# Kernel optimization log

Measured on AMD Instinct MI355X. Metric: run time of the kernel, lower is better.

Reference implementation:

```python
import jax, jax.numpy as jnp
import numpy as np

D_OUT = 256  # out_channels; fourier dim F = D_OUT (Wr has F/2 rows)

def _fourier_pos(H, W, Wr, w1, b1, w2, b2):
    # normalized (H,W) grid in [-1,1], shape [L,2]
    ys = jnp.linspace(-1.0, 1.0, H)
    xs = jnp.linspace(-1.0, 1.0, W)
    gy, gx = jnp.meshgrid(ys, xs, indexing='ij')
    grid = jnp.stack([gy, gx], axis=-1).reshape(-1, 2)  # [L,2]
    proj = grid @ Wr.T                                   # [L,F/2]
    F = 2 * Wr.shape[0]
    feats = jnp.concatenate([jnp.cos(proj), jnp.sin(proj)], axis=-1) / jnp.sqrt(jnp.float32(F))
    h = jax.nn.gelu(feats @ w1.T + b1)
    return h @ w2.T + b2                                 # [L,D_OUT]

def setup_inputs() -> dict:
    key = jax.random.key(0)
    ks = jax.random.split(key, 11)
    N, D, H, W = 16, 256, 128, 128
    s = 1.0 / np.sqrt(D)
    return {
        'x': jax.random.normal(ks[0], (N, D, H, W), jnp.float32),
        'query': jax.random.normal(ks[1], (D_OUT,), jnp.float32),
        'k_w': jax.random.normal(ks[2], (D_OUT, D), jnp.float32) * s,
        'k_b': jax.random.normal(ks[3], (D_OUT,), jnp.float32) * 0.01,
        'v_w': jax.random.normal(ks[4], (D_OUT, D), jnp.float32) * s,
        'v_b': jax.random.normal(ks[5], (D_OUT,), jnp.float32) * 0.01,
        'Wr': jax.random.normal(ks[6], (D_OUT // 2, 2), jnp.float32),
        'w1': jax.random.normal(ks[7], (D_OUT, D_OUT), jnp.float32) * (1.0 / np.sqrt(D_OUT)),
        'b1': jax.random.normal(ks[8], (D_OUT,), jnp.float32) * 0.01,
        'w2': jax.random.normal(ks[9], (D_OUT, D_OUT), jnp.float32) * (1.0 / np.sqrt(D_OUT)),
        'b2': jax.random.normal(ks[10], (D_OUT,), jnp.float32) * 0.01,
    }

def reference(x, query, k_w, k_b, v_w, v_b, Wr, w1, b1, w2, b2):
    N, D, H, W = x.shape
    L = H * W
    tok = x.reshape(N, D, L).transpose(0, 2, 1)          # [N,L,D]
    pos = _fourier_pos(H, W, Wr, w1, b1, w2, b2)         # [L,D_OUT]
    K = tok @ k_w.T + k_b + pos[None]                    # [N,L,D_OUT]
    V = tok @ v_w.T + v_b                                # [N,L,D_OUT]
    scores = jnp.einsum('nld,d->nl', K, query) / jnp.sqrt(jnp.float32(query.shape[0]))
    attn = jax.nn.softmax(scores, axis=1)                # [N,L]
    return jnp.einsum('nl,nld->nd', attn, V)             # [N,D_OUT]
```

## Files before the change

### kernel.cpp

```cpp
#include <hip/hip_runtime.h>
#include <math.h>

#define NB 16
#define DD 256
#define LL 16384
#define DO 256

#define WS_QK    0
#define WS_QW2   256
#define WS_C1    512
#define WS_C2    513
#define WS_W1T   768
#define WS_VWT   (WS_W1T + 65536)
#define WS_PQ    (WS_VWT + 65536)
#define WS_M     (WS_PQ + LL)
#define WS_DEN   (WS_M + NB*32)
#define WS_NUM   (WS_DEN + NB*32)

__device__ __forceinline__ float gelu_tanh(float u) {
    float u3 = u*u*u;
    return 0.5f*u*(1.0f + tanhf(0.7978845608028654f*(u + 0.044715f*u3)));
}

__global__ __launch_bounds__(256) void k0a(const float* __restrict__ query,
        const float* __restrict__ k_w, const float* __restrict__ k_b,
        const float* __restrict__ w2, const float* __restrict__ b2,
        float* __restrict__ ws) {
    __shared__ float q_s[DO];
    __shared__ float red[256];
    int t = threadIdx.x;
    q_s[t] = query[t];
    __syncthreads();
    float aqk = 0.f, aqw = 0.f;
    for (int o = 0; o < DO; ++o) {
        aqk += k_w[o*DD + t] * q_s[o];
        aqw += w2[o*DO + t] * q_s[o];
    }
    ws[WS_QK + t] = aqk;
    ws[WS_QW2 + t] = aqw;
    red[t] = k_b[t]*q_s[t];
    __syncthreads();
    for (int s = 128; s > 0; s >>= 1) { if (t < s) red[t] += red[t+s]; __syncthreads(); }
    if (t == 0) ws[WS_C1] = red[0];
    __syncthreads();
    red[t] = b2[t]*q_s[t];
    __syncthreads();
    for (int s = 128; s > 0; s >>= 1) { if (t < s) red[t] += red[t+s]; __syncthreads(); }
    if (t == 0) ws[WS_C2] = red[0];
}

__global__ __launch_bounds__(256) void k0b(const float* __restrict__ w1,
        const float* __restrict__ v_w, float* __restrict__ ws) {
    int t = threadIdx.x, b = blockIdx.x;
    if (b < 256) {
        ws[WS_W1T + b*DO + t] = w1[t*DO + b];
    } else {
        int c = b - 256;
        ws[WS_VWT + c*DO + t] = v_w[t*DD + c];
    }
}

__global__ __launch_bounds__(256) void k1_pq(const float* __restrict__ Wr,
        const float* __restrict__ b1, float* __restrict__ ws) {
    __shared__ float feats[32*256];
    __shared__ float wbuf[32*256];
    int t = threadIdx.x;
    int w = t >> 6, lane = t & 63;
    int l0 = blockIdx.x * 32;
    int r = t & 127;
    float wr0 = Wr[r*2], wr1 = Wr[r*2+1];
    bool is_cos = (t < 128);
    for (int lr = 0; lr < 32; ++lr) {
        int l = l0 + lr;
        int i = l >> 7, j = l & 127;
        float y = -1.0f + (2.0f/127.0f)*(float)i;
        float xg = -1.0f + (2.0f/127.0f)*(float)j;
        float p = y*wr0 + xg*wr1;
        feats[lr*256 + t] = (is_cos ? cosf(p) : sinf(p)) * 0.0625f;
    }
    int o4 = lane * 4;
    float z[8][4];
    #pragma unroll
    for (int a = 0; a < 8; ++a) { z[a][0]=0.f; z[a][1]=0.f; z[a][2]=0.f; z[a][3]=0.f; }
    __syncthreads();
    for (int fc = 0; fc < 8; ++fc) {
        #pragma unroll
        for (int i2 = 0; i2 < 8; ++i2) {
            int idx = i2*256 + t;
            int fl = idx >> 6;
            int c = (idx & 63) * 4;
            *(float4*)(wbuf + fl*256 + c) =
                *(const float4*)(ws + WS_W1T + (fc*32+fl)*DO + c);
        }
        __syncthreads();
        for (int f = 0; f < 32; ++f) {
            float4 wv = *(const float4*)(wbuf + f*256 + o4);
            #pragma unroll
            for (int lr = 0; lr < 8; ++lr) {
                float fv = feats[(w*8+lr)*256 + fc*32 + f];
                z[lr][0] += fv*wv.x; z[lr][1] += fv*wv.y;
                z[lr][2] += fv*wv.z; z[lr][3] += fv*wv.w;
            }
        }
        __syncthreads();
    }
    float4 b1v = *(const float4*)(b1 + o4);
    float4 qwv = *(const float4*)(ws + WS_QW2 + o4);
    float c2 = ws[WS_C2];
    #pragma unroll
    for (int lr = 0; lr < 8; ++lr) {
        float pp = gelu_tanh(z[lr][0]+b1v.x)*qwv.x + gelu_tanh(z[lr][1]+b1v.y)*qwv.y
                 + gelu_tanh(z[lr][2]+b1v.z)*qwv.z + gelu_tanh(z[lr][3]+b1v.w)*qwv.w;
        for (int off = 32; off > 0; off >>= 1) pp += __shfl_xor(pp, off);
        if (lane == 0) ws[WS_PQ + l0 + w*8 + lr] = pp + c2;
    }
}

__global__ __launch_bounds__(256) void k2_main(const float* __restrict__ x,
        float* __restrict__ ws) {
    __shared__ float tile[DD*65];
    __shared__ float qk_s[DD];
    __shared__ float e_s[64];
    __shared__ float part[256];
    __shared__ float m_s, den_s, sc_s;
    int t = threadIdx.x;
    int n = blockIdx.x >> 5, lb = blockIdx.x & 31;
    const float* xb = x + (size_t)n * DD * LL;
    qk_s[t] = ws[WS_QK + t];
    if (t == 0) { m_s = -INFINITY; den_s = 0.f; sc_s = 0.f; }
    float c1 = ws[WS_C1];
    float num = 0.f;
    int w = t >> 6, lane = t & 63;
    int dld = t >> 4;
    int li = (t & 15) * 4;
    for (int tb = 0; tb < 8; ++tb) {
        int l0 = lb*512 + tb*64;
        __syncthreads();
        #pragma unroll 4
        for (int i2 = 0; i2 < 16; ++i2) {
            int d = i2*16 + dld;
            float4 v = *(const float4*)(xb + (size_t)d*LL + l0 + li);
            float* dst = tile + d*65 + li;
            dst[0]=v.x; dst[1]=v.y; dst[2]=v.z; dst[3]=v.w;
        }
        __syncthreads();
        float acc = 0.f;
        int dbase = w*64;
        #pragma unroll 8
        for (int i2 = 0; i2 < 64; ++i2)
            acc += tile[(dbase+i2)*65 + lane] * qk_s[dbase+i2];
        part[t] = acc;
        __syncthreads();
        if (t < 64) {
            float dot = part[t] + part[64+t] + part[128+t] + part[192+t];
            float score = (dot + c1 + ws[WS_PQ + l0 + t]) * 0.0625f;
            float mc = score;
            for (int off=32; off>0; off>>=1) mc = fmaxf(mc, __shfl_xor(mc, off));
            float mold = m_s;
            float mnew = fmaxf(mold, mc);
            float e = expf(score - mnew);
            e_s[t] = e;
            float dc = e;
            for (int off=32; off>0; off>>=1) dc += __shfl_xor(dc, off);
            if (t == 0) {
                float sc = expf(mold - mnew);
                den_s = den_s*sc + dc;
                m_s = mnew;
                sc_s = sc;
            }
        }
        __syncthreads();
        float sc = sc_s;
        float acc2 = 0.f;
        #pragma unroll 8
        for (int l = 0; l < 64; ++l)
            acc2 += e_s[l] * tile[t*65 + l];
        num = num*sc + acc2;
    }
    int pb = n*32 + lb;
    ws[WS_NUM + pb*256 + t] = num;
    if (t == 0) { ws[WS_M + pb] = m_s; ws[WS_DEN + pb] = den_s; }
}

__global__ __launch_bounds__(256) void k3_final(const float* __restrict__ ws,
        const float* __restrict__ v_b, float* __restrict__ out) {
    __shared__ float s_s[DD];
    int t = threadIdx.x, n = blockIdx.x;
    float m = -INFINITY;
    for (int lb = 0; lb < 32; ++lb) m = fmaxf(m, ws[WS_M + n*32 + lb]);
    float den = 0.f;
    for (int lb = 0; lb < 32; ++lb)
        den += ws[WS_DEN + n*32 + lb] * expf(ws[WS_M + n*32 + lb] - m);
    float sacc = 0.f;
    for (int lb = 0; lb < 32; ++lb) {
        float sc = expf(ws[WS_M + n*32 + lb] - m);
        sacc += ws[WS_NUM + (n*32+lb)*256 + t] * sc;
    }
    s_s[t] = sacc / den;
    __syncthreads();
    float acc = v_b[t];
    for (int d = 0; d < DD; ++d)
        acc += ws[WS_VWT + d*DO + t] * s_s[d];
    out[n*DO + t] = acc;
}

extern "C" void kernel_launch(void* const* d_in, const int* in_sizes, int n_in,
                              void* d_out, int out_size, void* d_ws, size_t ws_size,
                              hipStream_t stream) {
    const float* x     = (const float*)d_in[0];
    const float* query = (const float*)d_in[1];
    const float* k_w   = (const float*)d_in[2];
    const float* k_b   = (const float*)d_in[3];
    const float* v_w   = (const float*)d_in[4];
    const float* v_b   = (const float*)d_in[5];
    const float* Wr    = (const float*)d_in[6];
    const float* w1    = (const float*)d_in[7];
    const float* b1    = (const float*)d_in[8];
    const float* w2    = (const float*)d_in[9];
    const float* b2    = (const float*)d_in[10];
    float* ws  = (float*)d_ws;
    float* out = (float*)d_out;

    k0a<<<1, 256, 0, stream>>>(query, k_w, k_b, w2, b2, ws);
    k0b<<<512, 256, 0, stream>>>(w1, v_w, ws);
    k1_pq<<<512, 256, 0, stream>>>(Wr, b1, ws);
    k2_main<<<512, 256, 0, stream>>>(x, ws);
    k3_final<<<16, 256, 0, stream>>>(ws, v_b, out);
}
```

Before: 477.8 us.

## Merge setup kernels, prefetch x tiles in registers, transpose Fourier features

The single-block query-projection kernel is folded into the weight-transpose kernel as 16 blocks that each write partial sums, which later kernels add up. The constant bias terms c1 and c2 are dropped because they shift every score equally and cancel in the softmax. The main kernel now loads the next 64-column x tile into registers while it computes on the current tile in shared memory, which hides global load latency at the cost of more registers. The Fourier feature buffer is stored transposed so the inner loop reads it with float4 loads, and a few loops gain unroll pragmas.

```diff
diff --git a/kernel.cpp b/kernel.cpp
--- a/kernel.cpp
+++ b/kernel.cpp
@@ -6,11 +6,9 @@
 #define LL 16384
 #define DO 256
 
-#define WS_QK    0
-#define WS_QW2   256
-#define WS_C1    512
-#define WS_C2    513
-#define WS_W1T   768
+#define WS_QKP   0
+#define WS_QW2P  2048
+#define WS_W1T   4096
 #define WS_VWT   (WS_W1T + 65536)
 #define WS_PQ    (WS_VWT + 65536)
 #define WS_M     (WS_PQ + LL)
@@ -22,67 +20,60 @@
     return 0.5f*u*(1.0f + tanhf(0.7978845608028654f*(u + 0.044715f*u3)));
 }
 
-__global__ __launch_bounds__(256) void k0a(const float* __restrict__ query,
-        const float* __restrict__ k_w, const float* __restrict__ k_b,
-        const float* __restrict__ w2, const float* __restrict__ b2,
+__global__ __launch_bounds__(256) void k0(const float* __restrict__ query,
+        const float* __restrict__ k_w, const float* __restrict__ w2,
+        const float* __restrict__ w1, const float* __restrict__ v_w,
         float* __restrict__ ws) {
-    __shared__ float q_s[DO];
-    __shared__ float red[256];
-    int t = threadIdx.x;
-    q_s[t] = query[t];
-    __syncthreads();
-    float aqk = 0.f, aqw = 0.f;
-    for (int o = 0; o < DO; ++o) {
-        aqk += k_w[o*DD + t] * q_s[o];
-        aqw += w2[o*DO + t] * q_s[o];
-    }
-    ws[WS_QK + t] = aqk;
-    ws[WS_QW2 + t] = aqw;
-    red[t] = k_b[t]*q_s[t];
-    __syncthreads();
-    for (int s = 128; s > 0; s >>= 1) { if (t < s) red[t] += red[t+s]; __syncthreads(); }
-    if (t == 0) ws[WS_C1] = red[0];
-    __syncthreads();
-    red[t] = b2[t]*q_s[t];
-    __syncthreads();
-    for (int s = 128; s > 0; s >>= 1) { if (t < s) red[t] += red[t+s]; __syncthreads(); }
-    if (t == 0) ws[WS_C2] = red[0];
-}
-
-__global__ __launch_bounds__(256) void k0b(const float* __restrict__ w1,
-        const float* __restrict__ v_w, float* __restrict__ ws) {
     int t = threadIdx.x, b = blockIdx.x;
-    if (b < 256) {
-        ws[WS_W1T + b*DO + t] = w1[t*DO + b];
+    if (b < 16) {
+        bool is_k = (b < 8);
+        int c = b & 7;
+        const float* M = is_k ? k_w : w2;
+        float a = 0.f;
+        #pragma unroll
+        for (int oi = 0; oi < 32; ++oi) {
+            int o = c*32 + oi;
+            a += M[o*DD + t] * query[o];
+        }
+        ws[(is_k ? WS_QKP : WS_QW2P) + c*256 + t] = a;
+    } else if (b < 272) {
+        int f = b - 16;
+        ws[WS_W1T + f*DO + t] = w1[t*DO + f];
     } else {
-        int c = b - 256;
-        ws[WS_VWT + c*DO + t] = v_w[t*DD + c];
+        int d = b - 272;
+        ws[WS_VWT + d*DO + t] = v_w[t*DD + d];
     }
 }
 
 __global__ __launch_bounds__(256) void k1_pq(const float* __restrict__ Wr,
         const float* __restrict__ b1, float* __restrict__ ws) {
-    __shared__ float feats[32*256];
-    __shared__ float wbuf[32*256];
+    __shared__ __align__(16) float featsT[256*36];
+    __shared__ __align__(16) float wbuf[32*256];
     int t = threadIdx.x;
     int w = t >> 6, lane = t & 63;
     int l0 = blockIdx.x * 32;
     int r = t & 127;
     float wr0 = Wr[r*2], wr1 = Wr[r*2+1];
     bool is_cos = (t < 128);
+    #pragma unroll 8
     for (int lr = 0; lr < 32; ++lr) {
         int l = l0 + lr;
         int i = l >> 7, j = l & 127;
         float y = -1.0f + (2.0f/127.0f)*(float)i;
         float xg = -1.0f + (2.0f/127.0f)*(float)j;
         float p = y*wr0 + xg*wr1;
-        feats[lr*256 + t] = (is_cos ? cosf(p) : sinf(p)) * 0.0625f;
+        featsT[t*36 + lr] = (is_cos ? cosf(p) : sinf(p)) * 0.0625f;
     }
     int o4 = lane * 4;
     float z[8][4];
     #pragma unroll
     for (int a = 0; a < 8; ++a) { z[a][0]=0.f; z[a][1]=0.f; z[a][2]=0.f; z[a][3]=0.f; }
-    __syncthreads();
+    float4 qwv; qwv.x = 0.f; qwv.y = 0.f; qwv.z = 0.f; qwv.w = 0.f;
+    #pragma unroll
+    for (int c = 0; c < 8; ++c) {
+        float4 p = *(const float4*)(ws + WS_QW2P + c*256 + o4);
+        qwv.x += p.x; qwv.y += p.y; qwv.z += p.z; qwv.w += p.w;
+    }
     for (int fc = 0; fc < 8; ++fc) {
         #pragma unroll
         for (int i2 = 0; i2 < 8; ++i2) {
@@ -93,32 +84,33 @@
                 *(const float4*)(ws + WS_W1T + (fc*32+fl)*DO + c);
         }
         __syncthreads();
-        for (int f = 0; f < 32; ++f) {
-            float4 wv = *(const float4*)(wbuf + f*256 + o4);
+        for (int fl = 0; fl < 32; ++fl) {
+            float4 wv = *(const float4*)(wbuf + fl*256 + o4);
+            const float* fr = featsT + (fc*32+fl)*36 + w*8;
+            float4 fa = *(const float4*)(fr);
+            float4 fb = *(const float4*)(fr+4);
+            float fv[8] = {fa.x,fa.y,fa.z,fa.w,fb.x,fb.y,fb.z,fb.w};
             #pragma unroll
             for (int lr = 0; lr < 8; ++lr) {
-                float fv = feats[(w*8+lr)*256 + fc*32 + f];
-                z[lr][0] += fv*wv.x; z[lr][1] += fv*wv.y;
-                z[lr][2] += fv*wv.z; z[lr][3] += fv*wv.w;
+                z[lr][0] += fv[lr]*wv.x; z[lr][1] += fv[lr]*wv.y;
+                z[lr][2] += fv[lr]*wv.z; z[lr][3] += fv[lr]*wv.w;
             }
         }
         __syncthreads();
     }
     float4 b1v = *(const float4*)(b1 + o4);
-    float4 qwv = *(const float4*)(ws + WS_QW2 + o4);
-    float c2 = ws[WS_C2];
     #pragma unroll
     for (int lr = 0; lr < 8; ++lr) {
         float pp = gelu_tanh(z[lr][0]+b1v.x)*qwv.x + gelu_tanh(z[lr][1]+b1v.y)*qwv.y
                  + gelu_tanh(z[lr][2]+b1v.z)*qwv.z + gelu_tanh(z[lr][3]+b1v.w)*qwv.w;
         for (int off = 32; off > 0; off >>= 1) pp += __shfl_xor(pp, off);
-        if (lane == 0) ws[WS_PQ + l0 + w*8 + lr] = pp + c2;
+        if (lane == 0) ws[WS_PQ + l0 + w*8 + lr] = pp;
     }
 }
 
 __global__ __launch_bounds__(256) void k2_main(const float* __restrict__ x,
         float* __restrict__ ws) {
-    __shared__ float tile[DD*65];
+    __shared__ __align__(16) float tile[DD*65];
     __shared__ float qk_s[DD];
     __shared__ float e_s[64];
     __shared__ float part[256];
@@ -126,24 +118,34 @@
     int t = threadIdx.x;
     int n = blockIdx.x >> 5, lb = blockIdx.x & 31;
     const float* xb = x + (size_t)n * DD * LL;
-    qk_s[t] = ws[WS_QK + t];
+    float aqk = 0.f;
+    #pragma unroll
+    for (int c = 0; c < 8; ++c) aqk += ws[WS_QKP + c*256 + t];
+    qk_s[t] = aqk;
     if (t == 0) { m_s = -INFINITY; den_s = 0.f; sc_s = 0.f; }
-    float c1 = ws[WS_C1];
     float num = 0.f;
     int w = t >> 6, lane = t & 63;
     int dld = t >> 4;
     int li = (t & 15) * 4;
+    float4 v[16];
+    #pragma unroll
+    for (int i2 = 0; i2 < 16; ++i2)
+        v[i2] = *(const float4*)(xb + (size_t)(i2*16 + dld)*LL + lb*512 + li);
+    __syncthreads();
+    #pragma unroll
+    for (int i2 = 0; i2 < 16; ++i2) {
+        float* dst = tile + (i2*16 + dld)*65 + li;
+        dst[0]=v[i2].x; dst[1]=v[i2].y; dst[2]=v[i2].z; dst[3]=v[i2].w;
+    }
+    __syncthreads();
     for (int tb = 0; tb < 8; ++tb) {
         int l0 = lb*512 + tb*64;
-        __syncthreads();
-        #pragma unroll 4
-        for (int i2 = 0; i2 < 16; ++i2) {
-            int d = i2*16 + dld;
-            float4 v = *(const float4*)(xb + (size_t)d*LL + l0 + li);
-            float* dst = tile + d*65 + li;
-            dst[0]=v.x; dst[1]=v.y; dst[2]=v.z; dst[3]=v.w;
-        }
-        __syncthreads();
+        if (tb < 7) {
+            int l0n = l0 + 64;
+            #pragma unroll
+            for (int i2 = 0; i2 < 16; ++i2)
+                v[i2] = *(const float4*)(xb + (size_t)(i2*16 + dld)*LL + l0n + li);
+        }
         float acc = 0.f;
         int dbase = w*64;
         #pragma unroll 8
@@ -153,7 +155,7 @@
         __syncthreads();
         if (t < 64) {
             float dot = part[t] + part[64+t] + part[128+t] + part[192+t];
-            float score = (dot + c1 + ws[WS_PQ + l0 + t]) * 0.0625f;
+            float score = (dot + ws[WS_PQ + l0 + t]) * 0.0625f;
             float mc = score;
             for (int off=32; off>0; off>>=1) mc = fmaxf(mc, __shfl_xor(mc, off));
             float mold = m_s;
@@ -176,6 +178,15 @@
         for (int l = 0; l < 64; ++l)
             acc2 += e_s[l] * tile[t*65 + l];
         num = num*sc + acc2;
+        __syncthreads();
+        if (tb < 7) {
+            #pragma unroll
+            for (int i2 = 0; i2 < 16; ++i2) {
+                float* dst = tile + (i2*16 + dld)*65 + li;
+                dst[0]=v[i2].x; dst[1]=v[i2].y; dst[2]=v[i2].z; dst[3]=v[i2].w;
+            }
+        }
+        __syncthreads();
     }
     int pb = n*32 + lb;
     ws[WS_NUM + pb*256 + t] = num;
@@ -187,11 +198,14 @@
     __shared__ float s_s[DD];
     int t = threadIdx.x, n = blockIdx.x;
     float m = -INFINITY;
+    #pragma unroll
     for (int lb = 0; lb < 32; ++lb) m = fmaxf(m, ws[WS_M + n*32 + lb]);
     float den = 0.f;
+    #pragma unroll
     for (int lb = 0; lb < 32; ++lb)
         den += ws[WS_DEN + n*32 + lb] * expf(ws[WS_M + n*32 + lb] - m);
     float sacc = 0.f;
+    #pragma unroll 4
     for (int lb = 0; lb < 32; ++lb) {
         float sc = expf(ws[WS_M + n*32 + lb] - m);
         sacc += ws[WS_NUM + (n*32+lb)*256 + t] * sc;
@@ -199,6 +213,7 @@
     s_s[t] = sacc / den;
     __syncthreads();
     float acc = v_b[t];
+    #pragma unroll 8
     for (int d = 0; d < DD; ++d)
         acc += ws[WS_VWT + d*DO + t] * s_s[d];
     out[n*DO + t] = acc;
@@ -210,19 +225,16 @@
     const float* x     = (const float*)d_in[0];
     const float* query = (const float*)d_in[1];
     const float* k_w   = (const float*)d_in[2];
-    const float* k_b   = (const float*)d_in[3];
     const float* v_w   = (const float*)d_in[4];
     const float* v_b   = (const float*)d_in[5];
     const float* Wr    = (const float*)d_in[6];
     const float* w1    = (const float*)d_in[7];
     const float* b1    = (const float*)d_in[8];
     const float* w2    = (const float*)d_in[9];
-    const float* b2    = (const float*)d_in[10];
     float* ws  = (float*)d_ws;
     float* out = (float*)d_out;
 
-    k0a<<<1, 256, 0, stream>>>(query, k_w, k_b, w2, b2, ws);
-    k0b<<<512, 256, 0, stream>>>(w1, v_w, ws);
+    k0<<<528, 256, 0, stream>>>(query, k_w, w2, w1, v_w, ws);
     k1_pq<<<512, 256, 0, stream>>>(Wr, b1, ws);
     k2_main<<<512, 256, 0, stream>>>(x, ws);
     k3_final<<<16, 256, 0, stream>>>(ws, v_b, out);
```

Result: faster. 446.7 us (-6.5%).
